# Optimization experiments

Hardware: AMD Instinct MI355X
Metric: run time of the kernel (lower is better)

Reference implementation:

```python
import jax, jax.numpy as jnp
import numpy as np

HIDDEN = 4096
HEAD_DIM = 128
N_HEADS = 32
N_KV_HEADS = 8
ROPE_THETA = 10000.0


def setup_inputs() -> dict:
    key = jax.random.key(0)
    k1, k2, k3 = jax.random.split(key, 3)
    qkv_dim = (N_HEADS + 2 * N_KV_HEADS) * HEAD_DIM  # 6144
    x = jax.random.normal(k1, (2, 2048, HIDDEN), dtype=jnp.float32)
    w_qkv = jax.random.normal(k2, (HIDDEN, qkv_dim), dtype=jnp.float32) * (HIDDEN ** -0.5)
    w_out = jax.random.normal(k3, (N_HEADS * HEAD_DIM, HIDDEN), dtype=jnp.float32) * ((N_HEADS * HEAD_DIM) ** -0.5)
    return {"x": x, "w_qkv": w_qkv, "w_out": w_out}


def _apply_rope(t):
    # t: [B, S, H, D], rotate over full head dim (half-split convention)
    B, S, H, D = t.shape
    half = D // 2
    inv_freq = 1.0 / (ROPE_THETA ** (jnp.arange(0, half, dtype=jnp.float32) / half))
    freqs = jnp.arange(S, dtype=jnp.float32)[:, None] * inv_freq[None, :]  # [S, D/2]
    cos = jnp.cos(freqs)[None, :, None, :].astype(t.dtype)
    sin = jnp.sin(freqs)[None, :, None, :].astype(t.dtype)
    t1, t2 = t[..., :half], t[..., half:]
    return jnp.concatenate([t1 * cos - t2 * sin, t1 * sin + t2 * cos], axis=-1)


def reference(x, w_qkv, w_out):
    B, S, _ = x.shape
    qkv = x @ w_qkv  # [B, S, (H + 2*Hkv) * D]
    qkv = qkv.reshape(B, S, N_HEADS + 2 * N_KV_HEADS, HEAD_DIM)
    q = qkv[:, :, :N_HEADS]                                 # [B,S,H,D]
    k = qkv[:, :, N_HEADS:N_HEADS + N_KV_HEADS]             # [B,S,Hkv,D]
    v = qkv[:, :, N_HEADS + N_KV_HEADS:]                    # [B,S,Hkv,D]
    q = _apply_rope(q)
    k = _apply_rope(k)
    # GQA: expand KV heads to match query heads
    group = N_HEADS // N_KV_HEADS
    k = jnp.repeat(k, group, axis=2)  # [B,S,H,D]
    v = jnp.repeat(v, group, axis=2)
    q = q.transpose(0, 2, 1, 3)  # [B,H,S,D]
    k = k.transpose(0, 2, 1, 3)
    v = v.transpose(0, 2, 1, 3)
    scale = HEAD_DIM ** -0.5
    scores = jnp.einsum('bhqd,bhkd->bhqk', q, k) * scale  # [B,H,S,S]
    probs = jax.nn.softmax(scores, axis=-1)
    out = jnp.einsum('bhqk,bhkd->bhqd', probs, v)  # [B,H,S,D]
    out = out.transpose(0, 2, 1, 3).reshape(B, S, N_HEADS * HEAD_DIM)
    return out @ w_out  # [B,S,hidden]
```

## Files before the change

kernel.cpp:

```cpp
#include <hip/hip_runtime.h>

typedef unsigned short u16;
typedef float f32x4 __attribute__((ext_vector_type(4)));
typedef __bf16 bf16x8 __attribute__((ext_vector_type(8)));

__device__ __forceinline__ u16 f2bf(float f) {
  union { float f; unsigned int u; } x; x.f = f;
  unsigned int u = x.u;
  u += 0x7fffu + ((u >> 16) & 1u);
  return (u16)(u >> 16);
}
__device__ __forceinline__ float bf2f(u16 h) {
  union { unsigned int u; float f; } x; x.u = ((unsigned int)h) << 16;
  return x.f;
}
#if __has_builtin(__builtin_amdgcn_exp2f)
__device__ __forceinline__ float exp2_hw(float x) { return __builtin_amdgcn_exp2f(x); }
#else
__device__ __forceinline__ float exp2_hw(float x) { return exp2f(x); }
#endif
__device__ __forceinline__ void load_lds16(const void* g, void* l) {
  __builtin_amdgcn_global_load_lds(
      (const __attribute__((address_space(1))) unsigned int*)g,
      (__attribute__((address_space(3))) unsigned int*)l, 16, 0, 0);
}
__device__ __forceinline__ f32x4 mfma16(bf16x8 a, bf16x8 b, f32x4 c) {
  return __builtin_amdgcn_mfma_f32_16x16x32_bf16(a, b, c, 0, 0, 0);
}
__device__ __forceinline__ void bar() { __builtin_amdgcn_s_barrier(); }
template <int Nw> __device__ __forceinline__ void waitvm() {
  if constexpr (Nw == 8)      asm volatile("s_waitcnt vmcnt(8)" ::: "memory");
  else if constexpr (Nw == 6) asm volatile("s_waitcnt vmcnt(6)" ::: "memory");
  else                        asm volatile("s_waitcnt vmcnt(0)" ::: "memory");
}

__global__ void convert4(const float* __restrict__ in, u16* __restrict__ out) {
  int i = blockIdx.x * blockDim.x + threadIdx.x;
  float4 v = reinterpret_cast<const float4*>(in)[i];
  ushort4 o;
  o.x = f2bf(v.x); o.y = f2bf(v.y); o.z = f2bf(v.z); o.w = f2bf(v.w);
  reinterpret_cast<ushort4*>(out)[i] = o;
}

__global__ void transpose_f32_bf16(const float* __restrict__ in, u16* __restrict__ out,
                                   int R, int Cd) {
  __shared__ float tile[32][33];
  int c0 = blockIdx.x * 32, r0 = blockIdx.y * 32;
  int tx = threadIdx.x, ty = threadIdx.y;
#pragma unroll
  for (int i = 0; i < 4; ++i)
    tile[ty + 8 * i][tx] = in[(size_t)(r0 + ty + 8 * i) * Cd + c0 + tx];
  __syncthreads();
#pragma unroll
  for (int i = 0; i < 4; ++i)
    out[(size_t)(c0 + ty + 8 * i) * R + r0 + tx] = f2bf(tile[tx][ty + 8 * i]);
}

__global__ void rope_table(float2* __restrict__ tab) {
  int i = blockIdx.x * blockDim.x + threadIdx.x;
  int s = i >> 6, d2 = i & 63;
  float inv = powf(10000.f, -(float)d2 * (1.f / 64.f));
  float fr = (float)s * inv;
  tab[i] = make_float2(cosf(fr), sinf(fr));
}

__global__ void rope_apply(u16* __restrict__ qkv, const float2* __restrict__ tab) {
  int i = blockIdx.x * blockDim.x + threadIdx.x;
  int d2 = i & 63;
  int head = (i >> 6) % 40;
  int row = i / 2560;
  size_t base = (size_t)row * 6144 + head * 128 + d2;
  float t1 = bf2f(qkv[base]), t2 = bf2f(qkv[base + 64]);
  float2 cs = tab[(row & 2047) * 64 + d2];
  float o1 = t1 * cs.x - t2 * cs.y;
  float o2 = t1 * cs.y + t2 * cs.x;
  float sc = (head < 32) ? 0.12751731654059898f : 1.f;
  qkv[base]      = f2bf(o1 * sc);
  qkv[base + 64] = f2bf(o2 * sc);
}

__global__ void build_vT(const u16* __restrict__ qkv, u16* __restrict__ vT) {
  __shared__ u16 tile[32][33];
  int st = blockIdx.x, dt = blockIdx.y, bh = blockIdx.z;
  int b = bh >> 3, hkv = bh & 7;
  int tx = threadIdx.x, ty = threadIdx.y;
  int s0 = st * 32, d0 = dt * 32;
#pragma unroll
  for (int i = 0; i < 4; ++i)
    tile[ty + 8 * i][tx] =
        qkv[(size_t)(b * 2048 + s0 + ty + 8 * i) * 6144 + 5120 + hkv * 128 + d0 + tx];
  __syncthreads();
  int s = s0 + tx;
  int sl = s & 63;
  int sp = (s & ~63) | (sl & 0x23) | ((sl & 0x0C) << 1) | ((sl & 0x10) >> 2);
#pragma unroll
  for (int i = 0; i < 4; ++i)
    vT[((size_t)bh * 128 + d0 + ty + 8 * i) * 2048 + sp] = tile[tx][ty + 8 * i];
}

template <int BM, int BN, int WM, int WN, int OUT_BF16>
__global__ __launch_bounds__(512, 2) void gemm8(const u16* __restrict__ A,
                                                const u16* __restrict__ BT,
                                                void* __restrict__ Cv,
                                                int M, int N, int K) {
  constexpr int WMS = BM / WM, WNS = BN / WN;
  constexpr int MF = WMS / 16;
  constexpr int A_OPS = BM / 64, B_OPS = BN / 64, TOT = A_OPS + B_OPS;
  constexpr int NP = (MF * (WNS / 16) * 2) / 16;
  static_assert(NP == 4 || NP == 2, "unsupported geometry");
  __shared__ u16 As[2][BM][64];
  __shared__ u16 Bs[2][BN][64];
  const int tid = threadIdx.x, lane = tid & 63, wave = tid >> 6;
  const int lr = lane & 15, lg = lane >> 4, l7 = lane & 7;
  const int wm = wave / WN, wn = wave % WN;
  const int nbx = N / BN;
  int bid = blockIdx.x;
  const int cpx = (int)gridDim.x >> 3;
  bid = (bid & 7) * cpx + (bid >> 3);
  const int bm = (bid / nbx) * BM, bn = (bid % nbx) * BN;
  const int NT = K / 64;
  const int ch0 = lg ^ l7, ch1 = (4 | lg) ^ l7;

  auto stageA = [&](int t) {
    int c2 = t & 1, k0 = t * 64;
#pragma unroll
    for (int o = 0; o < A_OPS; ++o) {
      int cid = o * 512 + tid;
      int row = cid >> 3;
      int sc2 = (cid & 7) ^ (row & 7);
      load_lds16(A + (size_t)(bm + row) * K + k0 + sc2 * 8,
                 (u16*)&As[c2][0][0] + (o * 512 + wave * 64) * 8);
    }
  };
  auto stageB = [&](int t) {
    int c2 = t & 1, k0 = t * 64;
#pragma unroll
    for (int o = 0; o < B_OPS; ++o) {
      int cid = o * 512 + tid;
      int row = cid >> 3;
      int sc2 = (cid & 7) ^ (row & 7);
      load_lds16(BT + (size_t)(bn + row) * K + k0 + sc2 * 8,
                 (u16*)&Bs[c2][0][0] + (o * 512 + wave * 64) * 8);
    }
  };

  f32x4 acc[MF][4];
#pragma unroll
  for (int i = 0; i < MF; ++i)
#pragma unroll
    for (int j = 0; j < 4; ++j) acc[i][j] = (f32x4){0.f, 0.f, 0.f, 0.f};

  stageB(0); stageA(0); stageB(1); stageA(1);
  waitvm<TOT>();
  bar();

  for (int t = 0; t < NT; ++t) {
    const int c = t & 1;
    const bool pf = (t + 2 < NT);
    bf16x8 af[4][2], bf[4][2];
    if constexpr (NP == 4) {
#pragma unroll
      for (int mi = 0; mi < 4; ++mi) {
        af[mi][0] = *(const bf16x8*)&As[c][wm * WMS + mi * 16 + lr][ch0 * 8];
        af[mi][1] = *(const bf16x8*)&As[c][wm * WMS + mi * 16 + lr][ch1 * 8];
      }
#pragma unroll
      for (int j = 0; j < 2; ++j) {
        bf[j][0] = *(const bf16x8*)&Bs[c][wn * WNS + j * 16 + lr][ch0 * 8];
        bf[j][1] = *(const bf16x8*)&Bs[c][wn * WNS + j * 16 + lr][ch1 * 8];
      }
      bar();
      __builtin_amdgcn_s_setprio(1);
#pragma unroll
      for (int mi = 0; mi < 4; ++mi)
#pragma unroll
        for (int j = 0; j < 2; ++j) {
          acc[mi][j] = mfma16(af[mi][0], bf[j][0], acc[mi][j]);
          acc[mi][j] = mfma16(af[mi][1], bf[j][1], acc[mi][j]);
        }
      __builtin_amdgcn_s_setprio(0);
      bar();
#pragma unroll
      for (int j = 2; j < 4; ++j) {
        bf[j][0] = *(const bf16x8*)&Bs[c][wn * WNS + j * 16 + lr][ch0 * 8];
        bf[j][1] = *(const bf16x8*)&Bs[c][wn * WNS + j * 16 + lr][ch1 * 8];
      }
      bar();
      __builtin_amdgcn_s_setprio(1);
#pragma unroll
      for (int mi = 0; mi < 4; ++mi)
#pragma unroll
        for (int j = 2; j < 4; ++j) {
          acc[mi][j] = mfma16(af[mi][0], bf[j][0], acc[mi][j]);
          acc[mi][j] = mfma16(af[mi][1], bf[j][1], acc[mi][j]);
        }
      __builtin_amdgcn_s_setprio(0);
      bar();
#pragma unroll
      for (int mi = 0; mi < 4; ++mi) {
        af[mi][0] = *(const bf16x8*)&As[c][wm * WMS + 64 + mi * 16 + lr][ch0 * 8];
        af[mi][1] = *(const bf16x8*)&As[c][wm * WMS + 64 + mi * 16 + lr][ch1 * 8];
      }
      if (pf) stageB(t + 2);
      bar();
      __builtin_amdgcn_s_setprio(1);
#pragma unroll
      for (int mi = 0; mi < 4; ++mi)
#pragma unroll
        for (int j = 0; j < 2; ++j) {
          acc[4 + mi][j] = mfma16(af[mi][0], bf[j][0], acc[4 + mi][j]);
          acc[4 + mi][j] = mfma16(af[mi][1], bf[j][1], acc[4 + mi][j]);
        }
      __builtin_amdgcn_s_setprio(0);
      bar();
      if (pf) stageA(t + 2);
      bar();
      __builtin_amdgcn_s_setprio(1);
#pragma unroll
      for (int mi = 0; mi < 4; ++mi)
#pragma unroll
        for (int j = 2; j < 4; ++j) {
          acc[4 + mi][j] = mfma16(af[mi][0], bf[j][0], acc[4 + mi][j]);
          acc[4 + mi][j] = mfma16(af[mi][1], bf[j][1], acc[4 + mi][j]);
        }
      __builtin_amdgcn_s_setprio(0);
      if (pf) waitvm<TOT>(); else waitvm<0>();
      bar();
    } else {
#pragma unroll
      for (int mi = 0; mi < 4; ++mi) {
        af[mi][0] = *(const bf16x8*)&As[c][wm * WMS + mi * 16 + lr][ch0 * 8];
        af[mi][1] = *(const bf16x8*)&As[c][wm * WMS + mi * 16 + lr][ch1 * 8];
      }
#pragma unroll
      for (int j = 0; j < 4; ++j) {
        bf[j][0] = *(const bf16x8*)&Bs[c][wn * WNS + j * 16 + lr][ch0 * 8];
        bf[j][1] = *(const bf16x8*)&Bs[c][wn * WNS + j * 16 + lr][ch1 * 8];
      }
      asm volatile("s_waitcnt lgkmcnt(0)" ::: "memory");
      bar();
      __builtin_amdgcn_s_setprio(1);
#pragma unroll
      for (int mi = 0; mi < 4; ++mi)
#pragma unroll
        for (int j = 0; j < 2; ++j) {
          acc[mi][j] = mfma16(af[mi][0], bf[j][0], acc[mi][j]);
          acc[mi][j] = mfma16(af[mi][1], bf[j][1], acc[mi][j]);
        }
      __builtin_amdgcn_s_setprio(0);
      bar();
      if (pf) { stageB(t + 2); stageA(t + 2); }
      bar();
      __builtin_amdgcn_s_setprio(1);
#pragma unroll
      for (int mi = 0; mi < 4; ++mi)
#pragma unroll
        for (int j = 2; j < 4; ++j) {
          acc[mi][j] = mfma16(af[mi][0], bf[j][0], acc[mi][j]);
          acc[mi][j] = mfma16(af[mi][1], bf[j][1], acc[mi][j]);
        }
      __builtin_amdgcn_s_setprio(0);
      if (pf) waitvm<TOT>(); else waitvm<0>();
      bar();
    }
  }

#pragma unroll
  for (int mi = 0; mi < MF; ++mi) {
    int row = bm + wm * WMS + (mi >> 2) * 64 + (mi & 3) * 16 + lg * 4;
#pragma unroll
    for (int j = 0; j < 4; ++j) {
      int col = bn + wn * WNS + j * 16 + lr;
#pragma unroll
      for (int r = 0; r < 4; ++r) {
        if constexpr (OUT_BF16)
          ((u16*)Cv)[(size_t)(row + r) * N + col] = f2bf(acc[mi][j][r]);
        else
          ((float*)Cv)[(size_t)(row + r) * N + col] = acc[mi][j][r];
      }
    }
  }
}

__global__ __launch_bounds__(256, 3) void attn_fused(const u16* __restrict__ qkv,
                                                     const u16* __restrict__ vT,
                                                     u16* __restrict__ attn_out) {
  __shared__ u16 Ksm[64][128];
  __shared__ u16 Vsm[128][64];
  const int qt = blockIdx.x, h = blockIdx.y, b = blockIdx.z;
  const int hkv = h >> 2;
  const int tid = threadIdx.x, lane = tid & 63, wave = tid >> 6;
  const int lr = lane & 15, lg = lane >> 4;
  const int qrow0 = qt * 128 + wave * 32;

  bf16x8 qf[2][4];
#pragma unroll
  for (int q2 = 0; q2 < 2; ++q2) {
    const u16* qp = qkv + (size_t)(b * 2048 + qrow0 + q2 * 16 + lr) * 6144 + h * 128;
#pragma unroll
    for (int kk = 0; kk < 4; ++kk)
      qf[q2][kk] = *(const bf16x8*)(qp + kk * 32 + lg * 8);
  }
  float l_acc[2] = {0.f, 0.f};
  f32x4 acc_o[2][8] = {};

  for (int kv0 = 0; kv0 < 2048; kv0 += 64) {
#pragma unroll
    for (int c = 0; c < 4; ++c) {
      int cid = c * 256 + tid;
      int base = (c * 256 + wave * 64) * 8;
      int krow = cid >> 4;
      int kcc = (cid & 15) ^ (krow & 7);
      load_lds16(qkv + (size_t)(b * 2048 + kv0 + krow) * 6144 + 4096 + hkv * 128 + kcc * 8,
                 (u16*)Ksm + base);
      int vrow = cid >> 3;
      int vcc = (cid & 7) ^ (vrow & 7);
      load_lds16(vT + ((size_t)(b * 8 + hkv) * 128 + vrow) * 2048 + kv0 + vcc * 8,
                 (u16*)Vsm + base);
    }
    __syncthreads();

    bf16x8 pfr[2][2];
#pragma unroll
    for (int k2 = 0; k2 < 2; ++k2) {
      f32x4 sc[2][2] = {};
#pragma unroll
      for (int ktl = 0; ktl < 2; ++ktl) {
        int krow = (k2 * 2 + ktl) * 16 + lr;
#pragma unroll
        for (int kk = 0; kk < 4; ++kk) {
          bf16x8 kf = *(const bf16x8*)((u16*)Ksm + krow * 128 +
                                       ((((kk << 2) | lg) ^ (krow & 7)) << 3));
          sc[0][ktl] = mfma16(kf, qf[0][kk], sc[0][ktl]);
          sc[1][ktl] = mfma16(kf, qf[1][kk], sc[1][ktl]);
        }
      }
#pragma unroll
      for (int q2 = 0; q2 < 2; ++q2) {
        bf16x8 pk;
#pragma unroll
        for (int ktl = 0; ktl < 2; ++ktl)
#pragma unroll
          for (int r = 0; r < 4; ++r) {
            float e = exp2_hw(sc[q2][ktl][r]);
            l_acc[q2] += e;
            pk[ktl * 4 + r] = (__bf16)e;
          }
        pfr[q2][k2] = pk;
      }
    }
#pragma unroll
    for (int dt = 0; dt < 8; ++dt) {
      int vrow = dt * 16 + lr;
#pragma unroll
      for (int k2 = 0; k2 < 2; ++k2) {
        bf16x8 vf = *(const bf16x8*)((u16*)Vsm + vrow * 64 +
                                     ((((k2 << 2) | lg) ^ (vrow & 7)) << 3));
        acc_o[0][dt] = mfma16(pfr[0][k2], vf, acc_o[0][dt]);
        acc_o[1][dt] = mfma16(pfr[1][k2], vf, acc_o[1][dt]);
      }
    }
    __syncthreads();
  }
#pragma unroll
  for (int q2 = 0; q2 < 2; ++q2) {
    float l = l_acc[q2];
    l += __shfl_xor(l, 16);
    l += __shfl_xor(l, 32);
    float li = 1.f / l;
    float linv[4];
#pragma unroll
    for (int r = 0; r < 4; ++r) linv[r] = __shfl(li, lg * 4 + r);
    u16* op = attn_out + (size_t)(b * 2048 + qrow0 + q2 * 16) * 4096 + h * 128;
#pragma unroll
    for (int dt = 0; dt < 8; ++dt)
#pragma unroll
      for (int r = 0; r < 4; ++r)
        op[(size_t)(lg * 4 + r) * 4096 + dt * 16 + lr] = f2bf(acc_o[q2][dt][r] * linv[r]);
  }
}

extern "C" void kernel_launch(void* const* d_in, const int* in_sizes, int n_in,
                              void* d_out, int out_size, void* d_ws, size_t ws_size,
                              hipStream_t stream) {
  const float* x     = (const float*)d_in[0];
  const float* w_qkv = (const float*)d_in[1];
  const float* w_out = (const float*)d_in[2];
  float* out = (float*)d_out;
  char* ws = (char*)d_ws;

  u16*    xbf = (u16*)(ws);
  u16*    wT  = (u16*)(ws + (size_t)33554432);
  u16*    qkv = (u16*)(ws + (size_t)83886080);
  u16*    vT  = (u16*)(ws + (size_t)134217728);
  float2* tab = (float2*)(ws + (size_t)142606336);

  dim3 tb(32, 8);
  convert4<<<16384, 256, 0, stream>>>(x, xbf);
  transpose_f32_bf16<<<dim3(192, 128), tb, 0, stream>>>(w_qkv, wT, 4096, 6144);
  rope_table<<<512, 256, 0, stream>>>(tab);
  gemm8<256, 128, 4, 2, 1><<<768, 512, 0, stream>>>(xbf, wT, qkv, 4096, 6144, 4096);
  rope_apply<<<40960, 256, 0, stream>>>(qkv, tab);
  build_vT<<<dim3(64, 4, 16), tb, 0, stream>>>(qkv, vT);
  attn_fused<<<dim3(16, 32, 2), 256, 0, stream>>>(qkv, vT, xbf);
  transpose_f32_bf16<<<dim3(128, 128), tb, 0, stream>>>(w_out, wT, 4096, 4096);
  gemm8<256, 256, 2, 4, 0><<<256, 512, 0, stream>>>(xbf, wT, out, 4096, 4096, 4096);
}
```

Baseline: 639.4 us.

## Software-pipeline LDS fragment loads across phases in both GEMM kernels

```diff
diff --git a/kernel.cpp b/kernel.cpp
--- a/kernel.cpp
+++ b/kernel.cpp
@@ -31,7 +31,28 @@
 template <int Nw> __device__ __forceinline__ void waitvm() {
   if constexpr (Nw == 8)      asm volatile("s_waitcnt vmcnt(8)" ::: "memory");
   else if constexpr (Nw == 6) asm volatile("s_waitcnt vmcnt(6)" ::: "memory");
+  else if constexpr (Nw == 4) asm volatile("s_waitcnt vmcnt(4)" ::: "memory");
   else                        asm volatile("s_waitcnt vmcnt(0)" ::: "memory");
+}
+__device__ __forceinline__ void phase_open() {
+  asm volatile("" ::: "memory");
+  __builtin_amdgcn_s_barrier();
+  asm volatile("s_waitcnt lgkmcnt(0)" ::: "memory");
+  __builtin_amdgcn_sched_barrier(0);
+  __builtin_amdgcn_s_setprio(1);
+}
+__device__ __forceinline__ void phase_close() {
+  __builtin_amdgcn_s_setprio(0);
+  asm volatile("" ::: "memory");
+  __builtin_amdgcn_s_barrier();
+  asm volatile("" ::: "memory");
+}
+template <int NV> __device__ __forceinline__ void phase_close_vm() {
+  __builtin_amdgcn_s_setprio(0);
+  asm volatile("" ::: "memory");
+  waitvm<NV>();
+  __builtin_amdgcn_s_barrier();
+  asm volatile("" ::: "memory");
 }
 
 __global__ void convert4(const float* __restrict__ in, u16* __restrict__ out) {
@@ -98,33 +119,28 @@
     vT[((size_t)bh * 128 + d0 + ty + 8 * i) * 2048 + sp] = tile[tx][ty + 8 * i];
 }
 
-template <int BM, int BN, int WM, int WN, int OUT_BF16>
-__global__ __launch_bounds__(512, 2) void gemm8(const u16* __restrict__ A,
-                                                const u16* __restrict__ BT,
-                                                void* __restrict__ Cv,
-                                                int M, int N, int K) {
-  constexpr int WMS = BM / WM, WNS = BN / WN;
-  constexpr int MF = WMS / 16;
-  constexpr int A_OPS = BM / 64, B_OPS = BN / 64, TOT = A_OPS + B_OPS;
-  constexpr int NP = (MF * (WNS / 16) * 2) / 16;
-  static_assert(NP == 4 || NP == 2, "unsupported geometry");
-  __shared__ u16 As[2][BM][64];
-  __shared__ u16 Bs[2][BN][64];
+template <int OUT_BF16>
+__global__ __launch_bounds__(512, 2) void gemm256x256(const u16* __restrict__ A,
+                                                      const u16* __restrict__ BT,
+                                                      void* __restrict__ Cv,
+                                                      int M, int N, int K) {
+  __shared__ u16 As[2][256][64];
+  __shared__ u16 Bs[2][256][64];
   const int tid = threadIdx.x, lane = tid & 63, wave = tid >> 6;
   const int lr = lane & 15, lg = lane >> 4, l7 = lane & 7;
-  const int wm = wave / WN, wn = wave % WN;
-  const int nbx = N / BN;
+  const int wm = wave >> 2, wn = wave & 3;
+  const int nbx = N / 256;
   int bid = blockIdx.x;
   const int cpx = (int)gridDim.x >> 3;
   bid = (bid & 7) * cpx + (bid >> 3);
-  const int bm = (bid / nbx) * BM, bn = (bid % nbx) * BN;
+  const int bm = (bid / nbx) * 256, bn = (bid % nbx) * 256;
   const int NT = K / 64;
-  const int ch0 = lg ^ l7, ch1 = (4 | lg) ^ l7;
+  const int ch0 = (lg ^ l7) << 3, ch1 = ((4 | lg) ^ l7) << 3;
 
   auto stageA = [&](int t) {
     int c2 = t & 1, k0 = t * 64;
 #pragma unroll
-    for (int o = 0; o < A_OPS; ++o) {
+    for (int o = 0; o < 4; ++o) {
       int cid = o * 512 + tid;
       int row = cid >> 3;
       int sc2 = (cid & 7) ^ (row & 7);
@@ -135,7 +151,7 @@
   auto stageB = [&](int t) {
     int c2 = t & 1, k0 = t * 64;
 #pragma unroll
-    for (int o = 0; o < B_OPS; ++o) {
+    for (int o = 0; o < 4; ++o) {
       int cid = o * 512 + tid;
       int row = cid >> 3;
       int sc2 = (cid & 7) ^ (row & 7);
@@ -144,133 +160,210 @@
     }
   };
 
-  f32x4 acc[MF][4];
-#pragma unroll
-  for (int i = 0; i < MF; ++i)
-#pragma unroll
-    for (int j = 0; j < 4; ++j) acc[i][j] = (f32x4){0.f, 0.f, 0.f, 0.f};
-
-  stageB(0); stageA(0); stageB(1); stageA(1);
-  waitvm<TOT>();
+  bf16x8 a0[4][2], a1[4][2], b01[2][2], b23[2][2];
+  f32x4 acc[8][4] = {};
+
+  stageA(0); stageB(0); stageA(1); stageB(1);
+  waitvm<8>();
   bar();
+#pragma unroll
+  for (int mi = 0; mi < 4; ++mi) {
+    a0[mi][0] = *(const bf16x8*)&As[0][wm * 128 + mi * 16 + lr][ch0];
+    a0[mi][1] = *(const bf16x8*)&As[0][wm * 128 + mi * 16 + lr][ch1];
+  }
+#pragma unroll
+  for (int j = 0; j < 2; ++j) {
+    b01[j][0] = *(const bf16x8*)&Bs[0][wn * 64 + j * 16 + lr][ch0];
+    b01[j][1] = *(const bf16x8*)&Bs[0][wn * 64 + j * 16 + lr][ch1];
+  }
 
   for (int t = 0; t < NT; ++t) {
-    const int c = t & 1;
-    const bool pf = (t + 2 < NT);
-    bf16x8 af[4][2], bf[4][2];
-    if constexpr (NP == 4) {
-#pragma unroll
-      for (int mi = 0; mi < 4; ++mi) {
-        af[mi][0] = *(const bf16x8*)&As[c][wm * WMS + mi * 16 + lr][ch0 * 8];
-        af[mi][1] = *(const bf16x8*)&As[c][wm * WMS + mi * 16 + lr][ch1 * 8];
-      }
+    const int c = t & 1, cn = c ^ 1;
+    const bool pf = (t + 2) < NT;
+#pragma unroll
+    for (int j = 0; j < 2; ++j) {
+      b23[j][0] = *(const bf16x8*)&Bs[c][wn * 64 + (j + 2) * 16 + lr][ch0];
+      b23[j][1] = *(const bf16x8*)&Bs[c][wn * 64 + (j + 2) * 16 + lr][ch1];
+    }
+    phase_open();
+#pragma unroll
+    for (int mi = 0; mi < 4; ++mi)
 #pragma unroll
       for (int j = 0; j < 2; ++j) {
-        bf[j][0] = *(const bf16x8*)&Bs[c][wn * WNS + j * 16 + lr][ch0 * 8];
-        bf[j][1] = *(const bf16x8*)&Bs[c][wn * WNS + j * 16 + lr][ch1 * 8];
-      }
-      bar();
-      __builtin_amdgcn_s_setprio(1);
-#pragma unroll
-      for (int mi = 0; mi < 4; ++mi)
-#pragma unroll
-        for (int j = 0; j < 2; ++j) {
-          acc[mi][j] = mfma16(af[mi][0], bf[j][0], acc[mi][j]);
-          acc[mi][j] = mfma16(af[mi][1], bf[j][1], acc[mi][j]);
-        }
-      __builtin_amdgcn_s_setprio(0);
-      bar();
-#pragma unroll
-      for (int j = 2; j < 4; ++j) {
-        bf[j][0] = *(const bf16x8*)&Bs[c][wn * WNS + j * 16 + lr][ch0 * 8];
-        bf[j][1] = *(const bf16x8*)&Bs[c][wn * WNS + j * 16 + lr][ch1 * 8];
-      }
-      bar();
-      __builtin_amdgcn_s_setprio(1);
-#pragma unroll
-      for (int mi = 0; mi < 4; ++mi)
-#pragma unroll
-        for (int j = 2; j < 4; ++j) {
-          acc[mi][j] = mfma16(af[mi][0], bf[j][0], acc[mi][j]);
-          acc[mi][j] = mfma16(af[mi][1], bf[j][1], acc[mi][j]);
-        }
-      __builtin_amdgcn_s_setprio(0);
-      bar();
-#pragma unroll
-      for (int mi = 0; mi < 4; ++mi) {
-        af[mi][0] = *(const bf16x8*)&As[c][wm * WMS + 64 + mi * 16 + lr][ch0 * 8];
-        af[mi][1] = *(const bf16x8*)&As[c][wm * WMS + 64 + mi * 16 + lr][ch1 * 8];
-      }
-      if (pf) stageB(t + 2);
-      bar();
-      __builtin_amdgcn_s_setprio(1);
-#pragma unroll
-      for (int mi = 0; mi < 4; ++mi)
-#pragma unroll
-        for (int j = 0; j < 2; ++j) {
-          acc[4 + mi][j] = mfma16(af[mi][0], bf[j][0], acc[4 + mi][j]);
-          acc[4 + mi][j] = mfma16(af[mi][1], bf[j][1], acc[4 + mi][j]);
-        }
-      __builtin_amdgcn_s_setprio(0);
-      bar();
-      if (pf) stageA(t + 2);
-      bar();
-      __builtin_amdgcn_s_setprio(1);
-#pragma unroll
-      for (int mi = 0; mi < 4; ++mi)
-#pragma unroll
-        for (int j = 2; j < 4; ++j) {
-          acc[4 + mi][j] = mfma16(af[mi][0], bf[j][0], acc[4 + mi][j]);
-          acc[4 + mi][j] = mfma16(af[mi][1], bf[j][1], acc[4 + mi][j]);
-        }
-      __builtin_amdgcn_s_setprio(0);
-      if (pf) waitvm<TOT>(); else waitvm<0>();
-      bar();
-    } else {
-#pragma unroll
-      for (int mi = 0; mi < 4; ++mi) {
-        af[mi][0] = *(const bf16x8*)&As[c][wm * WMS + mi * 16 + lr][ch0 * 8];
-        af[mi][1] = *(const bf16x8*)&As[c][wm * WMS + mi * 16 + lr][ch1 * 8];
-      }
-#pragma unroll
-      for (int j = 0; j < 4; ++j) {
-        bf[j][0] = *(const bf16x8*)&Bs[c][wn * WNS + j * 16 + lr][ch0 * 8];
-        bf[j][1] = *(const bf16x8*)&Bs[c][wn * WNS + j * 16 + lr][ch1 * 8];
-      }
-      asm volatile("s_waitcnt lgkmcnt(0)" ::: "memory");
-      bar();
-      __builtin_amdgcn_s_setprio(1);
-#pragma unroll
-      for (int mi = 0; mi < 4; ++mi)
-#pragma unroll
-        for (int j = 0; j < 2; ++j) {
-          acc[mi][j] = mfma16(af[mi][0], bf[j][0], acc[mi][j]);
-          acc[mi][j] = mfma16(af[mi][1], bf[j][1], acc[mi][j]);
-        }
-      __builtin_amdgcn_s_setprio(0);
-      bar();
-      if (pf) { stageB(t + 2); stageA(t + 2); }
-      bar();
-      __builtin_amdgcn_s_setprio(1);
-#pragma unroll
-      for (int mi = 0; mi < 4; ++mi)
-#pragma unroll
-        for (int j = 2; j < 4; ++j) {
-          acc[mi][j] = mfma16(af[mi][0], bf[j][0], acc[mi][j]);
-          acc[mi][j] = mfma16(af[mi][1], bf[j][1], acc[mi][j]);
-        }
-      __builtin_amdgcn_s_setprio(0);
-      if (pf) waitvm<TOT>(); else waitvm<0>();
-      bar();
-    }
-  }
-
-#pragma unroll
-  for (int mi = 0; mi < MF; ++mi) {
-    int row = bm + wm * WMS + (mi >> 2) * 64 + (mi & 3) * 16 + lg * 4;
+        acc[mi][j] = mfma16(a0[mi][0], b01[j][0], acc[mi][j]);
+        acc[mi][j] = mfma16(a0[mi][1], b01[j][1], acc[mi][j]);
+      }
+    phase_close();
+#pragma unroll
+    for (int mi = 0; mi < 4; ++mi) {
+      a1[mi][0] = *(const bf16x8*)&As[c][wm * 128 + 64 + mi * 16 + lr][ch0];
+      a1[mi][1] = *(const bf16x8*)&As[c][wm * 128 + 64 + mi * 16 + lr][ch1];
+    }
+    if (pf) stageB(t + 2);
+    phase_open();
+#pragma unroll
+    for (int mi = 0; mi < 4; ++mi)
+#pragma unroll
+      for (int j = 0; j < 2; ++j) {
+        acc[mi][j + 2] = mfma16(a0[mi][0], b23[j][0], acc[mi][j + 2]);
+        acc[mi][j + 2] = mfma16(a0[mi][1], b23[j][1], acc[mi][j + 2]);
+      }
+    if (pf) phase_close_vm<4>(); else phase_close_vm<0>();
+#pragma unroll
+    for (int mi = 0; mi < 4; ++mi) {
+      a0[mi][0] = *(const bf16x8*)&As[cn][wm * 128 + mi * 16 + lr][ch0];
+      a0[mi][1] = *(const bf16x8*)&As[cn][wm * 128 + mi * 16 + lr][ch1];
+    }
+    if (pf) stageA(t + 2);
+    phase_open();
+#pragma unroll
+    for (int mi = 0; mi < 4; ++mi)
+#pragma unroll
+      for (int j = 0; j < 2; ++j) {
+        acc[mi + 4][j] = mfma16(a1[mi][0], b01[j][0], acc[mi + 4][j]);
+        acc[mi + 4][j] = mfma16(a1[mi][1], b01[j][1], acc[mi + 4][j]);
+      }
+    phase_close();
+#pragma unroll
+    for (int j = 0; j < 2; ++j) {
+      b01[j][0] = *(const bf16x8*)&Bs[cn][wn * 64 + j * 16 + lr][ch0];
+      b01[j][1] = *(const bf16x8*)&Bs[cn][wn * 64 + j * 16 + lr][ch1];
+    }
+    phase_open();
+#pragma unroll
+    for (int mi = 0; mi < 4; ++mi)
+#pragma unroll
+      for (int j = 0; j < 2; ++j) {
+        acc[mi + 4][j + 2] = mfma16(a1[mi][0], b23[j][0], acc[mi + 4][j + 2]);
+        acc[mi + 4][j + 2] = mfma16(a1[mi][1], b23[j][1], acc[mi + 4][j + 2]);
+      }
+    phase_close();
+  }
+#pragma unroll
+  for (int mi = 0; mi < 8; ++mi) {
+    int row = bm + wm * 128 + mi * 16 + lg * 4;
 #pragma unroll
     for (int j = 0; j < 4; ++j) {
-      int col = bn + wn * WNS + j * 16 + lr;
+      int col = bn + wn * 64 + j * 16 + lr;
+#pragma unroll
+      for (int r = 0; r < 4; ++r) {
+        if constexpr (OUT_BF16)
+          ((u16*)Cv)[(size_t)(row + r) * N + col] = f2bf(acc[mi][j][r]);
+        else
+          ((float*)Cv)[(size_t)(row + r) * N + col] = acc[mi][j][r];
+      }
+    }
+  }
+}
+
+#define G1_TILE(T, C, CUR, NXT)                                               \
+  {                                                                           \
+    const bool pf = ((T) + 2) < NT;                                           \
+    _Pragma("unroll")                                                         \
+    for (int j = 0; j < 2; ++j) {                                             \
+      b23[j][0] = *(const bf16x8*)&Bs[C][wn * 64 + (j + 2) * 16 + lr][ch0];   \
+      b23[j][1] = *(const bf16x8*)&Bs[C][wn * 64 + (j + 2) * 16 + lr][ch1];   \
+    }                                                                         \
+    if (pf) stageA((T) + 2);                                                  \
+    phase_open();                                                             \
+    _Pragma("unroll")                                                         \
+    for (int mi = 0; mi < 4; ++mi)                                            \
+      _Pragma("unroll")                                                       \
+      for (int j = 0; j < 2; ++j) {                                           \
+        acc[mi][j] = mfma16(CUR[mi][0], b01[j][0], acc[mi][j]);               \
+        acc[mi][j] = mfma16(CUR[mi][1], b01[j][1], acc[mi][j]);               \
+      }                                                                       \
+    if (pf) phase_close_vm<4>(); else phase_close_vm<0>();                    \
+    _Pragma("unroll")                                                         \
+    for (int mi = 0; mi < 4; ++mi) {                                          \
+      NXT[mi][0] = *(const bf16x8*)&As[(C) ^ 1][wm * 64 + mi * 16 + lr][ch0]; \
+      NXT[mi][1] = *(const bf16x8*)&As[(C) ^ 1][wm * 64 + mi * 16 + lr][ch1]; \
+    }                                                                         \
+    _Pragma("unroll")                                                         \
+    for (int j = 0; j < 2; ++j) {                                             \
+      b01[j][0] = *(const bf16x8*)&Bs[(C) ^ 1][wn * 64 + j * 16 + lr][ch0];   \
+      b01[j][1] = *(const bf16x8*)&Bs[(C) ^ 1][wn * 64 + j * 16 + lr][ch1];   \
+    }                                                                         \
+    if (pf) stageB((T) + 2);                                                  \
+    phase_open();                                                             \
+    _Pragma("unroll")                                                         \
+    for (int mi = 0; mi < 4; ++mi)                                            \
+      _Pragma("unroll")                                                       \
+      for (int j = 0; j < 2; ++j) {                                           \
+        acc[mi][j + 2] = mfma16(CUR[mi][0], b23[j][0], acc[mi][j + 2]);       \
+        acc[mi][j + 2] = mfma16(CUR[mi][1], b23[j][1], acc[mi][j + 2]);       \
+      }                                                                       \
+    phase_close();                                                            \
+  }
+
+template <int OUT_BF16>
+__global__ __launch_bounds__(512, 2) void gemm256x128(const u16* __restrict__ A,
+                                                      const u16* __restrict__ BT,
+                                                      void* __restrict__ Cv,
+                                                      int M, int N, int K) {
+  __shared__ u16 As[2][256][64];
+  __shared__ u16 Bs[2][128][64];
+  const int tid = threadIdx.x, lane = tid & 63, wave = tid >> 6;
+  const int lr = lane & 15, lg = lane >> 4, l7 = lane & 7;
+  const int wm = wave >> 1, wn = wave & 1;
+  const int nbx = N / 128;
+  int bid = blockIdx.x;
+  const int cpx = (int)gridDim.x >> 3;
+  bid = (bid & 7) * cpx + (bid >> 3);
+  const int bm = (bid / nbx) * 256, bn = (bid % nbx) * 128;
+  const int NT = K / 64;
+  const int ch0 = (lg ^ l7) << 3, ch1 = ((4 | lg) ^ l7) << 3;
+
+  auto stageA = [&](int t) {
+    int c2 = t & 1, k0 = t * 64;
+#pragma unroll
+    for (int o = 0; o < 4; ++o) {
+      int cid = o * 512 + tid;
+      int row = cid >> 3;
+      int sc2 = (cid & 7) ^ (row & 7);
+      load_lds16(A + (size_t)(bm + row) * K + k0 + sc2 * 8,
+                 (u16*)&As[c2][0][0] + (o * 512 + wave * 64) * 8);
+    }
+  };
+  auto stageB = [&](int t) {
+    int c2 = t & 1, k0 = t * 64;
+#pragma unroll
+    for (int o = 0; o < 2; ++o) {
+      int cid = o * 512 + tid;
+      int row = cid >> 3;
+      int sc2 = (cid & 7) ^ (row & 7);
+      load_lds16(BT + (size_t)(bn + row) * K + k0 + sc2 * 8,
+                 (u16*)&Bs[c2][0][0] + (o * 512 + wave * 64) * 8);
+    }
+  };
+
+  bf16x8 Aa[4][2], Ab[4][2], b01[2][2], b23[2][2];
+  f32x4 acc[4][4] = {};
+
+  stageA(0); stageB(0); stageA(1); stageB(1);
+  waitvm<6>();
+  bar();
+#pragma unroll
+  for (int mi = 0; mi < 4; ++mi) {
+    Aa[mi][0] = *(const bf16x8*)&As[0][wm * 64 + mi * 16 + lr][ch0];
+    Aa[mi][1] = *(const bf16x8*)&As[0][wm * 64 + mi * 16 + lr][ch1];
+  }
+#pragma unroll
+  for (int j = 0; j < 2; ++j) {
+    b01[j][0] = *(const bf16x8*)&Bs[0][wn * 64 + j * 16 + lr][ch0];
+    b01[j][1] = *(const bf16x8*)&Bs[0][wn * 64 + j * 16 + lr][ch1];
+  }
+
+  for (int tt = 0; tt < NT; tt += 2) {
+    G1_TILE(tt, 0, Aa, Ab);
+    G1_TILE(tt + 1, 1, Ab, Aa);
+  }
+#pragma unroll
+  for (int mi = 0; mi < 4; ++mi) {
+    int row = bm + wm * 64 + mi * 16 + lg * 4;
+#pragma unroll
+    for (int j = 0; j < 4; ++j) {
+      int col = bn + wn * 64 + j * 16 + lr;
 #pragma unroll
       for (int r = 0; r < 4; ++r) {
         if constexpr (OUT_BF16)
@@ -399,10 +492,10 @@
   convert4<<<16384, 256, 0, stream>>>(x, xbf);
   transpose_f32_bf16<<<dim3(192, 128), tb, 0, stream>>>(w_qkv, wT, 4096, 6144);
   rope_table<<<512, 256, 0, stream>>>(tab);
-  gemm8<256, 128, 4, 2, 1><<<768, 512, 0, stream>>>(xbf, wT, qkv, 4096, 6144, 4096);
+  gemm256x128<1><<<768, 512, 0, stream>>>(xbf, wT, qkv, 4096, 6144, 4096);
   rope_apply<<<40960, 256, 0, stream>>>(qkv, tab);
   build_vT<<<dim3(64, 4, 16), tb, 0, stream>>>(qkv, vT);
   attn_fused<<<dim3(16, 32, 2), 256, 0, stream>>>(qkv, vT, xbf);
   transpose_f32_bf16<<<dim3(128, 128), tb, 0, stream>>>(w_out, wT, 4096, 4096);
-  gemm8<256, 256, 2, 4, 0><<<256, 512, 0, stream>>>(xbf, wT, out, 4096, 4096, 4096);
-}
+  gemm256x256<0><<<256, 512, 0, stream>>>(xbf, wT, out, 4096, 4096, 4096);
+}
```

New measurement: 626.5 us. 1.02x faster.
